# Optimization experiments

Measured on AMD Instinct MI355X. Metric: run time of the kernel, lower is better.

Reference implementation:

```python
import jax, jax.numpy as jnp
import numpy as np

B, S, E, H, L = 4, 8192, 1024, 16, 64
D = E // H

def setup_inputs() -> dict:
    key = jax.random.key(0)
    ks = jax.random.split(key, 8)
    scale = 1.0 / np.sqrt(E)
    inp = {
        'query': jax.random.normal(ks[0], (B, S, E), jnp.float32),
        'key':   jax.random.normal(ks[1], (B, S, E), jnp.float32),
        'value': jax.random.normal(ks[2], (B, S, E), jnp.float32),
        'Wq': jax.random.normal(ks[3], (E, E), jnp.float32) * scale,
        'bq': jnp.zeros((E,), jnp.float32),
        'Wk': jax.random.normal(ks[4], (E, E), jnp.float32) * scale,
        'bk': jnp.zeros((E,), jnp.float32),
        'Wv': jax.random.normal(ks[5], (E, E), jnp.float32) * scale,
        'bv': jnp.zeros((E,), jnp.float32),
        'Wo': jax.random.normal(ks[6], (E, E), jnp.float32) * scale,
        'bo': jnp.zeros((E,), jnp.float32),
    }
    return inp

def reference(query, key, value, Wq, bq, Wk, bk, Wv, bv, Wo, bo):
    b, s, _ = query.shape
    # projections (torch Linear: x @ W.T + b), split heads -> [B, H, S, D]
    def split(x):
        return x.reshape(b, s, H, D).transpose(0, 2, 1, 3)
    q = split(query @ Wq.T + bq)
    k = split(key   @ Wk.T + bk)
    v = split(value @ Wv.T + bv)
    # landmark selection: key-norms averaged over heads -> [B, S], topk L per batch
    scores = jnp.linalg.norm(k, axis=-1).mean(axis=1)        # [B, S]
    _, idx = jax.lax.top_k(scores, L)                        # [B, L]
    # gather landmark K/V -> [B, H, L, D]
    gidx = idx[:, None, :, None]                             # [B, 1, L, 1]
    k_sp = jnp.take_along_axis(k, gidx, axis=2)
    v_sp = jnp.take_along_axis(v, gidx, axis=2)
    # attention over landmarks only
    attn = jnp.einsum('bhsd,bhld->bhsl', q, k_sp) / jnp.sqrt(jnp.asarray(D, q.dtype))
    w = jax.nn.softmax(attn, axis=-1)                        # [B, H, S, L]
    out = jnp.einsum('bhsl,bhld->bhsd', w, v_sp)             # [B, H, S, D]
    out = out.transpose(0, 2, 1, 3).reshape(b, s, E)
    out = out @ Wo.T + bo
    return (out, w)
```

## Files before the change

### kernel.cpp

```cpp
#include <hip/hip_runtime.h>
#include <cstdint>

typedef unsigned short u16;
typedef __attribute__((ext_vector_type(8))) short short8;
typedef __attribute__((ext_vector_type(4))) float f32x4;

#define AS1 __attribute__((address_space(1)))
#define AS3 __attribute__((address_space(3)))

#define BB 4
#define SS 8192
#define EE 1024
#define HH 16
#define DD 64
#define LL 64
#define CANDN 96

__device__ __forceinline__ void async16(const void* g, void* l) {
  __builtin_amdgcn_global_load_lds((const AS1 uint32_t*)g, (AS3 uint32_t*)l, 16, 0, 0);
}
__device__ __forceinline__ u16 f2b(float f) {
  uint32_t u = __float_as_uint(f);
  return (u16)((u + 0x7fffu + ((u >> 16) & 1u)) >> 16);
}
__device__ __forceinline__ float b2f(u16 h) { return __uint_as_float(((uint32_t)h) << 16); }

__global__ __launch_bounds__(256) void cvt_bf16_k(const float* __restrict__ in, u16* __restrict__ out, int n4) {
  int i = blockIdx.x * 256 + threadIdx.x;
  if (i >= n4) return;
  float4 v = ((const float4*)in)[i];
  ushort4 o;
  o.x = f2b(v.x); o.y = f2b(v.y); o.z = f2b(v.z); o.w = f2b(v.w);
  ((ushort4*)out)[i] = o;
}

__global__ __launch_bounds__(256) void gemm_bt(const u16* __restrict__ A, const u16* __restrict__ W,
                                               const float* __restrict__ bias,
                                               float* __restrict__ Cf, u16* __restrict__ Cb, int K) {
  __shared__ __align__(16) u16 lA[4096];
  __shared__ __align__(16) u16 lB[4096];
  const int tid = threadIdx.x;
  const int wv = tid >> 6, lane = tid & 63;
  const int quad = lane >> 4, l15 = lane & 15;
  const int wm = wv >> 1, wn = wv & 1;

  const int nwg = gridDim.x * gridDim.y;
  int g = blockIdx.y * gridDim.x + blockIdx.x;
  int bx = blockIdx.x, by = blockIdx.y;
  if ((nwg & 7) == 0) {
    const int chunk = nwg >> 3;
    const int v = (g & 7) * chunk + (g >> 3);
    bx = v % gridDim.x;
    by = v / gridDim.x;
  }
  const int mt = by * 128, nt = bx * 128;

  const int row0 = tid >> 2, cg0 = (tid & 3) ^ ((row0 >> 1) & 3);
  const int row1 = (256 + tid) >> 2, cg1 = (tid & 3) ^ ((row1 >> 1) & 3);
  const u16* gA0 = A + (size_t)(mt + row0) * K + cg0 * 8;
  const u16* gA1 = A + (size_t)(mt + row1) * K + cg1 * 8;
  const u16* gB0 = W + (size_t)(nt + row0) * K + cg0 * 8;
  const u16* gB1 = W + (size_t)(nt + row1) * K + cg1 * 8;
  u16* lA0 = lA + tid * 8;  u16* lA1 = lA + 2048 + tid * 8;
  u16* lB0 = lB + tid * 8;  u16* lB1 = lB + 2048 + tid * 8;

  f32x4 acc[4][4];
#pragma unroll
  for (int i = 0; i < 4; i++)
#pragma unroll
    for (int j = 0; j < 4; j++) acc[i][j] = (f32x4){0.f, 0.f, 0.f, 0.f};

  const int am = 64 * wm + l15;
  const int bn = 64 * wn + l15;

  for (int kt = 0; kt < K; kt += 32) {
    async16(gA0 + kt, lA0);
    async16(gA1 + kt, lA1);
    async16(gB0 + kt, lB0);
    async16(gB1 + kt, lB1);
    __syncthreads();
    short8 af[4], bfr[4];
#pragma unroll
    for (int i = 0; i < 4; i++) {
      int r = am + 16 * i;
      af[i] = ((const short8*)lA)[r * 4 + (quad ^ ((r >> 1) & 3))];
      int rn = bn + 16 * i;
      bfr[i] = ((const short8*)lB)[rn * 4 + (quad ^ ((rn >> 1) & 3))];
    }
#pragma unroll
    for (int i = 0; i < 4; i++)
#pragma unroll
      for (int j = 0; j < 4; j++)
        acc[i][j] = __builtin_amdgcn_mfma_f32_16x16x32_bf16(af[i], bfr[j], acc[i][j], 0, 0, 0);
    __syncthreads();
  }

#pragma unroll
  for (int j = 0; j < 4; j++) {
    int gn = nt + 64 * wn + 16 * j + l15;
    float bs = bias[gn];
#pragma unroll
    for (int i = 0; i < 4; i++) {
#pragma unroll
      for (int r = 0; r < 4; r++) {
        int gm = mt + 64 * wm + 16 * i + quad * 4 + r;
        float v = acc[i][j][r] + bs;
        if (Cf) Cf[(size_t)gm * EE + gn] = v;
        if (Cb) Cb[(size_t)gm * EE + gn] = f2b(v);
      }
    }
  }
}

__global__ __launch_bounds__(256) void scores_k(const u16* __restrict__ kb, float* __restrict__ sc) {
  const int row = blockIdx.x;
  const int wv = threadIdx.x >> 6, lane = threadIdx.x & 63;
  __shared__ float part[4];
  float acc = 0.f;
  const u16* base = kb + (size_t)row * EE;
#pragma unroll
  for (int hh = 0; hh < 4; hh++) {
    float v = b2f(base[(wv * 4 + hh) * 64 + lane]);
    float s = v * v;
#pragma unroll
    for (int m = 1; m < 64; m <<= 1) s += __shfl_xor(s, m, 64);
    acc += sqrtf(s);
  }
  if (lane == 0) part[wv] = acc;
  __syncthreads();
  if (threadIdx.x == 0) sc[row] = (part[0] + part[1] + part[2] + part[3]) * (1.f / 16.f);
}

#define TKT 1024
#define EQCAP 256
__global__ __launch_bounds__(TKT) void topk1_k(const float* __restrict__ sc, int* __restrict__ cand) {
  const int b = blockIdx.x;
  __shared__ uint32_t s[SS];
  __shared__ int wsum[TKT / 64];
  __shared__ int cnt_sh;
  __shared__ int counter, eqcount;
  __shared__ int eqbuf[EQCAP];
  const int tid = threadIdx.x;
  const int lane = tid & 63, wv = tid >> 6;
  for (int i = tid; i < SS; i += TKT) s[i] = __float_as_uint(sc[b * SS + i]);
  if (tid == 0) { counter = 0; eqcount = 0; }
  __syncthreads();

  uint32_t lo = 0u, hi = 0x7f7fffffu;
  while (lo < hi) {
    uint32_t mid = lo + ((hi - lo + 1) >> 1);
    int c = 0;
    for (int i = tid; i < SS; i += TKT) c += (s[i] >= mid) ? 1 : 0;
#pragma unroll
    for (int m = 1; m < 64; m <<= 1) c += __shfl_xor(c, m, 64);
    if (lane == 0) wsum[wv] = c;
    __syncthreads();
    if (tid == 0) {
      int t = 0;
#pragma unroll
      for (int w = 0; w < TKT / 64; w++) t += wsum[w];
      cnt_sh = t;
    }
    __syncthreads();
    if (cnt_sh >= CANDN) lo = mid; else hi = mid - 1;
    __syncthreads();
  }
  const uint32_t T = lo;

  for (int i = tid; i < SS; i += TKT) {
    uint32_t u = s[i];
    if (u > T) {
      int p = atomicAdd(&counter, 1);
      cand[b * CANDN + p] = i;
    } else if (u == T) {
      int p = atomicAdd(&eqcount, 1);
      if (p < EQCAP) eqbuf[p] = i;
    }
  }
  __syncthreads();
  const int above = counter;
  const int rem = CANDN - above;
  int ec = eqcount; if (ec > EQCAP) ec = EQCAP;
  __syncthreads();
  for (int i = tid; i < ec; i += TKT) {
    int me = eqbuf[i];
    int rank = 0;
    for (int j = 0; j < ec; j++) rank += (eqbuf[j] < me) ? 1 : 0;
    if (rank < rem) {
      int p = atomicAdd(&counter, 1);
      cand[b * CANDN + p] = me;
    }
  }
}

__global__ __launch_bounds__(256) void rescore_k(const float* __restrict__ key, const float* __restrict__ Wk,
                                                 const int* __restrict__ cand, double* __restrict__ kpart) {
  const int kc = blockIdx.x, h = blockIdx.y, b = blockIdx.z;
  const int d = threadIdx.x & 63, cg = threadIdx.x >> 6;
  __shared__ float wk[64 * 257];
  __shared__ float xs[24 * 256];
  for (int i = threadIdx.x; i < 64 * 256; i += 256)
    wk[(i >> 8) * 257 + (i & 255)] = Wk[(size_t)(h * 64 + (i >> 8)) * EE + kc * 256 + (i & 255)];
  for (int c0 = 0; c0 < CANDN; c0 += 24) {
    __syncthreads();
    for (int i = threadIdx.x; i < 24 * 256; i += 256) {
      int c = c0 + (i >> 8);
      xs[i] = key[((size_t)b * SS + cand[b * CANDN + c]) * EE + kc * 256 + (i & 255)];
    }
    __syncthreads();
    double acc[6] = {0, 0, 0, 0, 0, 0};
    for (int kk = 0; kk < 256; kk++) {
      double wv_ = (double)wk[d * 257 + kk];
#pragma unroll
      for (int j = 0; j < 6; j++)
        acc[j] += wv_ * (double)xs[(cg * 6 + j) * 256 + kk];
    }
#pragma unroll
    for (int j = 0; j < 6; j++) {
      int c = c0 + cg * 6 + j;
      kpart[(((size_t)kc * BB + b) * CANDN + c) * 1024 + h * 64 + d] = acc[j];
    }
  }
}

__global__ __launch_bounds__(64) void score2_k(const double* __restrict__ kpart, const float* __restrict__ bk,
                                               double* __restrict__ sc2) {
  const int c = blockIdx.x, b = blockIdx.y;
  const int lane = threadIdx.x;
  double tot = 0.0;
  for (int h = 0; h < HH; h++) {
    double v = (double)bk[h * 64 + lane];
#pragma unroll
    for (int kc = 0; kc < 4; kc++)
      v += kpart[(((size_t)kc * BB + b) * CANDN + c) * 1024 + h * 64 + lane];
    double s = v * v;
#pragma unroll
    for (int m = 1; m < 64; m <<= 1) s += __shfl_xor(s, m, 64);
    tot += sqrt(s);
  }
  if (lane == 0) sc2[b * CANDN + c] = tot * (1.0 / 16.0);
}

__global__ __launch_bounds__(128) void topk2_k(const double* __restrict__ sc2, const int* __restrict__ cand,
                                               int* __restrict__ idxf) {
  const int b = blockIdx.x, t = threadIdx.x;
  if (t >= CANDN) return;
  double my = sc2[b * CANDN + t];
  int mi = cand[b * CANDN + t];
  int rank = 0;
  for (int j = 0; j < CANDN; j++) {
    double sj = sc2[b * CANDN + j];
    int ij = cand[b * CANDN + j];
    if (sj > my || (sj == my && ij < mi)) rank++;
  }
  if (rank < LL) idxf[b * LL + rank] = mi;
}

__global__ __launch_bounds__(256) void gatherx_k(const float* __restrict__ value, const int* __restrict__ idxf,
                                                 u16* __restrict__ xg) {
  const int r = blockIdx.x;
  const int b = r >> 6;
  const float* src = value + ((size_t)b * SS + idxf[r]) * EE;
  for (int i = threadIdx.x; i < EE; i += 256) xg[(size_t)r * EE + i] = f2b(src[i]);
}

__global__ __launch_bounds__(64) void gathersp_k(const u16* __restrict__ kb, const float* __restrict__ vg,
                                                 const int* __restrict__ idxf,
                                                 u16* __restrict__ ksp, u16* __restrict__ vspT) {
  const int g = blockIdx.x;
  const int l = g & 63, h = (g >> 6) & 15, b = g >> 10;
  const int d = threadIdx.x;
  ksp[(size_t)g * 64 + d] = kb[((size_t)b * SS + idxf[b * 64 + l]) * EE + h * 64 + d];
  vspT[((size_t)(b * 16 + h) * 64 + d) * 64 + l] = f2b(vg[((size_t)b * 64 + l) * EE + h * 64 + d]);
}

__global__ __launch_bounds__(256) void attn_k(const u16* __restrict__ qb, const u16* __restrict__ ksp,
                                              const u16* __restrict__ vspT,
                                              float* __restrict__ wout, u16* __restrict__ attnb) {
  __shared__ __align__(16) u16 qt[4096];
  __shared__ __align__(16) u16 kt[4096];
  __shared__ __align__(16) u16 vt[4096];
  __shared__ __align__(16) u16 wt[4096];
  const int tid = threadIdx.x;
  const int wv = tid >> 6, lane = tid & 63, quad = lane >> 4, l15 = lane & 15;
  const int s0 = blockIdx.x * 64;
  const int bh = blockIdx.y, b = bh >> 4, h = bh & 15;

  {
    const int bi0 = tid, bi1 = 256 + tid;
    const int r0 = bi0 >> 3, c0 = (bi0 & 7) ^ (r0 & 7);
    const int r1 = bi1 >> 3, c1 = (bi1 & 7) ^ (r1 & 7);
    const u16* qg = qb + ((size_t)b * SS + s0) * EE + h * 64;
    async16(qg + (size_t)r0 * EE + c0 * 8, qt + bi0 * 8);
    async16(qg + (size_t)r1 * EE + c1 * 8, qt + bi1 * 8);
    const u16* kg = ksp + (size_t)bh * 4096;
    async16(kg + r0 * 64 + c0 * 8, kt + bi0 * 8);
    async16(kg + r1 * 64 + c1 * 8, kt + bi1 * 8);
    const u16* vgp = vspT + (size_t)bh * 4096;
    async16(vgp + r0 * 64 + c0 * 8, vt + bi0 * 8);
    async16(vgp + r1 * 64 + c1 * 8, vt + bi1 * 8);
  }
  __syncthreads();

  f32x4 acc[4];
#pragma unroll
  for (int j = 0; j < 4; j++) acc[j] = (f32x4){0.f, 0.f, 0.f, 0.f};
  const int ar = 16 * wv + l15;
#pragma unroll
  for (int ks = 0; ks < 2; ks++) {
    const int cg = quad + ks * 4;
    short8 af = ((const short8*)qt)[ar * 8 + (cg ^ (ar & 7))];
#pragma unroll
    for (int j = 0; j < 4; j++) {
      int br = 16 * j + l15;
      short8 bf = ((const short8*)kt)[br * 8 + (cg ^ (br & 7))];
      acc[j] = __builtin_amdgcn_mfma_f32_16x16x32_bf16(af, bf, acc[j], 0, 0, 0);
    }
  }
#pragma unroll
  for (int j = 0; j < 4; j++) acc[j] *= 0.125f;

  float inv[4];
#pragma unroll
  for (int r = 0; r < 4; r++) {
    float m = fmaxf(fmaxf(acc[0][r], acc[1][r]), fmaxf(acc[2][r], acc[3][r]));
#pragma unroll
    for (int msk = 1; msk < 16; msk <<= 1) m = fmaxf(m, __shfl_xor(m, msk, 64));
    float e0 = __expf(acc[0][r] - m);
    float e1 = __expf(acc[1][r] - m);
    float e2 = __expf(acc[2][r] - m);
    float e3 = __expf(acc[3][r] - m);
    acc[0][r] = e0; acc[1][r] = e1; acc[2][r] = e2; acc[3][r] = e3;
    float s = e0 + e1 + e2 + e3;
#pragma unroll
    for (int msk = 1; msk < 16; msk <<= 1) s += __shfl_xor(s, msk, 64);
    inv[r] = 1.f / s;
  }

  const size_t wbase = ((size_t)bh * SS + s0 + 16 * wv) * 64;
#pragma unroll
  for (int j = 0; j < 4; j++) {
#pragma unroll
    for (int r = 0; r < 4; r++) {
      float val = acc[j][r] * inv[r];
      int rowl = quad * 4 + r;
      int l = 16 * j + l15;
      wout[wbase + (size_t)rowl * 64 + l] = val;
      int wr = 16 * wv + rowl;
      wt[wr * 64 + ((l >> 3) ^ (wr & 7)) * 8 + (l & 7)] = f2b(val);
    }
  }
  __syncthreads();

  f32x4 acc2[4];
#pragma unroll
  for (int j = 0; j < 4; j++) acc2[j] = (f32x4){0.f, 0.f, 0.f, 0.f};
#pragma unroll
  for (int ks = 0; ks < 2; ks++) {
    const int cg = quad + ks * 4;
    short8 af = ((const short8*)wt)[ar * 8 + (cg ^ (ar & 7))];
#pragma unroll
    for (int j = 0; j < 4; j++) {
      int br = 16 * j + l15;
      short8 bf = ((const short8*)vt)[br * 8 + (cg ^ (br & 7))];
      acc2[j] = __builtin_amdgcn_mfma_f32_16x16x32_bf16(af, bf, acc2[j], 0, 0, 0);
    }
  }
#pragma unroll
  for (int j = 0; j < 4; j++)
#pragma unroll
    for (int r = 0; r < 4; r++)
      attnb[((size_t)b * SS + s0 + 16 * wv + quad * 4 + r) * EE + h * 64 + 16 * j + l15] = f2b(acc2[j][r]);
}

extern "C" void kernel_launch(void* const* d_in, const int* in_sizes, int n_in,
                              void* d_out, int out_size, void* d_ws, size_t ws_size,
                              hipStream_t stream) {
  (void)in_sizes; (void)n_in; (void)out_size; (void)ws_size;
  const float* query = (const float*)d_in[0];
  const float* key   = (const float*)d_in[1];
  const float* value = (const float*)d_in[2];
  const float* Wq = (const float*)d_in[3];
  const float* bq = (const float*)d_in[4];
  const float* Wk = (const float*)d_in[5];
  const float* bk = (const float*)d_in[6];
  const float* Wv = (const float*)d_in[7];
  const float* bv = (const float*)d_in[8];
  const float* Wo = (const float*)d_in[9];
  const float* bo = (const float*)d_in[10];
  float* out = (float*)d_out;
  float* wout = out + (size_t)BB * SS * EE;

  char* p = (char*)d_ws;
  auto alloc = [&](size_t n) { char* r = p; p += (n + 255) & ~(size_t)255; return r; };
  u16* qbf = (u16*)alloc((size_t)BB * SS * EE * 2);
  u16* kbf = (u16*)alloc((size_t)BB * SS * EE * 2);
  u16* wqb = (u16*)alloc((size_t)EE * EE * 2);
  u16* wkb = (u16*)alloc((size_t)EE * EE * 2);
  u16* wvb = (u16*)alloc((size_t)EE * EE * 2);
  u16* wob = (u16*)alloc((size_t)EE * EE * 2);
  u16* qb  = (u16*)alloc((size_t)BB * SS * EE * 2);
  u16* kb  = (u16*)alloc((size_t)BB * SS * EE * 2);
  float*  sc    = (float*)alloc((size_t)BB * SS * 4);
  int*    cand  = (int*)alloc(BB * CANDN * 4);
  double* kpart = (double*)alloc((size_t)4 * BB * CANDN * 1024 * 8);
  double* sc2   = (double*)alloc(BB * CANDN * 8);
  int*    idxf  = (int*)alloc(BB * LL * 4);
  u16*    xg    = (u16*)alloc((size_t)BB * LL * EE * 2);
  float*  vg    = (float*)alloc((size_t)BB * LL * EE * 4);
  u16*    ksp   = (u16*)alloc((size_t)BB * HH * LL * DD * 2);
  u16*    vspT  = (u16*)alloc((size_t)BB * HH * DD * LL * 2);
  u16*    attnb = qbf;

  const int M = BB * SS;

  cvt_bf16_k<<<(M * EE / 4 + 255) / 256, 256, 0, stream>>>(query, qbf, M * EE / 4);
  cvt_bf16_k<<<(M * EE / 4 + 255) / 256, 256, 0, stream>>>(key, kbf, M * EE / 4);
  cvt_bf16_k<<<(EE * EE / 4 + 255) / 256, 256, 0, stream>>>(Wq, wqb, EE * EE / 4);
  cvt_bf16_k<<<(EE * EE / 4 + 255) / 256, 256, 0, stream>>>(Wk, wkb, EE * EE / 4);
  cvt_bf16_k<<<(EE * EE / 4 + 255) / 256, 256, 0, stream>>>(Wv, wvb, EE * EE / 4);
  cvt_bf16_k<<<(EE * EE / 4 + 255) / 256, 256, 0, stream>>>(Wo, wob, EE * EE / 4);

  dim3 gg(EE / 128, M / 128);
  gemm_bt<<<gg, 256, 0, stream>>>(qbf, wqb, bq, nullptr, qb, EE);
  gemm_bt<<<gg, 256, 0, stream>>>(kbf, wkb, bk, nullptr, kb, EE);

  scores_k<<<M, 256, 0, stream>>>(kb, sc);
  topk1_k<<<BB, TKT, 0, stream>>>(sc, cand);
  rescore_k<<<dim3(4, HH, BB), 256, 0, stream>>>(key, Wk, cand, kpart);
  score2_k<<<dim3(CANDN, BB), 64, 0, stream>>>(kpart, bk, sc2);
  topk2_k<<<BB, 128, 0, stream>>>(sc2, cand, idxf);

  gatherx_k<<<BB * LL, 256, 0, stream>>>(value, idxf, xg);
  gemm_bt<<<dim3(EE / 128, BB * LL / 128), 256, 0, stream>>>(xg, wvb, bv, vg, nullptr, EE);
  gathersp_k<<<BB * HH * LL, 64, 0, stream>>>(kb, vg, idxf, ksp, vspT);

  attn_k<<<dim3(SS / 64, BB * HH), 256, 0, stream>>>(qb, ksp, vspT, wout, attnb);

  gemm_bt<<<gg, 256, 0, stream>>>(attnb, wob, bo, out, nullptr, EE);
}
```

Baseline: 1.077 ms.

## Replace GEMM with double-buffered 256x128 tile, 512-thread, K64 pipelined kernel

New measurement: 1.006 ms. 1.07x faster.

```diff
diff --git a/kernel.cpp b/kernel.cpp
--- a/kernel.cpp
+++ b/kernel.cpp
@@ -34,11 +34,16 @@
   ((ushort4*)out)[i] = o;
 }
 
-__global__ __launch_bounds__(256) void gemm_bt(const u16* __restrict__ A, const u16* __restrict__ W,
+#define FENCE_RW()  asm volatile("s_waitcnt lgkmcnt(0)\n\ts_barrier" ::: "memory")
+#define FENCE_V6()  asm volatile("s_waitcnt vmcnt(6)\n\ts_barrier" ::: "memory")
+#define FENCE_V0()  asm volatile("s_waitcnt vmcnt(0)\n\ts_barrier" ::: "memory")
+
+__global__ __launch_bounds__(512) void gemm256(const u16* __restrict__ A, const u16* __restrict__ W,
                                                const float* __restrict__ bias,
                                                float* __restrict__ Cf, u16* __restrict__ Cb, int K) {
-  __shared__ __align__(16) u16 lA[4096];
-  __shared__ __align__(16) u16 lB[4096];
+  extern __shared__ __align__(16) u16 lds_[];
+  u16* lA = lds_;
+  u16* lB = lds_ + 32768;
   const int tid = threadIdx.x;
   const int wv = tid >> 6, lane = tid & 63;
   const int quad = lane >> 4, l15 = lane & 15;
@@ -53,16 +58,28 @@
     bx = v % gridDim.x;
     by = v / gridDim.x;
   }
-  const int mt = by * 128, nt = bx * 128;
-
-  const int row0 = tid >> 2, cg0 = (tid & 3) ^ ((row0 >> 1) & 3);
-  const int row1 = (256 + tid) >> 2, cg1 = (tid & 3) ^ ((row1 >> 1) & 3);
-  const u16* gA0 = A + (size_t)(mt + row0) * K + cg0 * 8;
-  const u16* gA1 = A + (size_t)(mt + row1) * K + cg1 * 8;
-  const u16* gB0 = W + (size_t)(nt + row0) * K + cg0 * 8;
-  const u16* gB1 = W + (size_t)(nt + row1) * K + cg1 * 8;
-  u16* lA0 = lA + tid * 8;  u16* lA1 = lA + 2048 + tid * 8;
-  u16* lB0 = lB + tid * 8;  u16* lB1 = lB + 2048 + tid * 8;
+  const int mt = by * 256, nt = bx * 128;
+
+  const int rl = tid >> 3;
+  const int g8 = (((tid & 7) ^ (rl & 7))) * 8;
+  const u16* sA00 = A + (size_t)(mt + rl) * K + g8;
+  const u16* sA01 = A + (size_t)(mt + 64 + rl) * K + g8;
+  const u16* sA10 = A + (size_t)(mt + 128 + rl) * K + g8;
+  const u16* sA11 = A + (size_t)(mt + 192 + rl) * K + g8;
+  const u16* sB0  = W + (size_t)(nt + rl) * K + g8;
+  const u16* sB1  = W + (size_t)(nt + 64 + rl) * K + g8;
+  const int dA = tid * 8;
+  const int dB = tid * 8;
+
+  auto STAGE = [&](int tile, int pb) {
+    const int off = tile * 64;
+    async16(sA00 + off, lA + pb * 16384 + dA);
+    async16(sA01 + off, lA + pb * 16384 + dA + 4096);
+    async16(sA10 + off, lA + pb * 16384 + 8192 + dA);
+    async16(sA11 + off, lA + pb * 16384 + 8192 + dA + 4096);
+    async16(sB0 + off, lB + pb * 8192 + dB);
+    async16(sB1 + off, lB + pb * 8192 + dB + 4096);
+  };
 
   f32x4 acc[4][4];
 #pragma unroll
@@ -70,29 +87,40 @@
 #pragma unroll
     for (int j = 0; j < 4; j++) acc[i][j] = (f32x4){0.f, 0.f, 0.f, 0.f};
 
-  const int am = 64 * wm + l15;
-  const int bn = 64 * wn + l15;
-
-  for (int kt = 0; kt < K; kt += 32) {
-    async16(gA0 + kt, lA0);
-    async16(gA1 + kt, lA1);
-    async16(gB0 + kt, lB0);
-    async16(gB1 + kt, lB1);
-    __syncthreads();
-    short8 af[4], bfr[4];
+  const int NT = K >> 6;
+  STAGE(0, 0);
+  STAGE(1, 1);
+  FENCE_V6();
+
+  for (int t = 0; t < NT; ++t) {
+    const int pb = t & 1;
+    const short8* pA = (const short8*)(lA + pb * 16384);
+    const short8* pB = (const short8*)(lB + pb * 8192);
+    short8 af[2][4], bf[2][4];
 #pragma unroll
     for (int i = 0; i < 4; i++) {
-      int r = am + 16 * i;
-      af[i] = ((const short8*)lA)[r * 4 + (quad ^ ((r >> 1) & 3))];
-      int rn = bn + 16 * i;
-      bfr[i] = ((const short8*)lB)[rn * 4 + (quad ^ ((rn >> 1) & 3))];
+      const int r = 64 * wm + 16 * i + l15;
+      af[0][i] = pA[r * 8 + (quad ^ (r & 7))];
+      af[1][i] = pA[r * 8 + ((quad + 4) ^ (r & 7))];
+      const int rb = 64 * wn + 16 * i + l15;
+      bf[0][i] = pB[rb * 8 + (quad ^ (rb & 7))];
+      bf[1][i] = pB[rb * 8 + ((quad + 4) ^ (rb & 7))];
     }
 #pragma unroll
     for (int i = 0; i < 4; i++)
 #pragma unroll
       for (int j = 0; j < 4; j++)
-        acc[i][j] = __builtin_amdgcn_mfma_f32_16x16x32_bf16(af[i], bfr[j], acc[i][j], 0, 0, 0);
-    __syncthreads();
+        acc[i][j] = __builtin_amdgcn_mfma_f32_16x16x32_bf16(af[0][i], bf[0][j], acc[i][j], 0, 0, 0);
+    FENCE_RW();
+    if (t + 2 < NT) STAGE(t + 2, pb);
+#pragma unroll
+    for (int i = 0; i < 4; i++)
+#pragma unroll
+      for (int j = 0; j < 4; j++)
+        acc[i][j] = __builtin_amdgcn_mfma_f32_16x16x32_bf16(af[1][i], bf[1][j], acc[i][j], 0, 0, 0);
+    if (t + 1 < NT) {
+      if (t + 1 == NT - 1) { FENCE_V0(); } else { FENCE_V6(); }
+    }
   }
 
 #pragma unroll
@@ -413,6 +441,7 @@
   u16*    attnb = qbf;
 
   const int M = BB * SS;
+  const size_t gemm_lds = 98304;
 
   cvt_bf16_k<<<(M * EE / 4 + 255) / 256, 256, 0, stream>>>(query, qbf, M * EE / 4);
   cvt_bf16_k<<<(M * EE / 4 + 255) / 256, 256, 0, stream>>>(key, kbf, M * EE / 4);
@@ -421,9 +450,9 @@
   cvt_bf16_k<<<(EE * EE / 4 + 255) / 256, 256, 0, stream>>>(Wv, wvb, EE * EE / 4);
   cvt_bf16_k<<<(EE * EE / 4 + 255) / 256, 256, 0, stream>>>(Wo, wob, EE * EE / 4);
 
-  dim3 gg(EE / 128, M / 128);
-  gemm_bt<<<gg, 256, 0, stream>>>(qbf, wqb, bq, nullptr, qb, EE);
-  gemm_bt<<<gg, 256, 0, stream>>>(kbf, wkb, bk, nullptr, kb, EE);
+  dim3 gg(EE / 128, M / 256);
+  gemm256<<<gg, 512, gemm_lds, stream>>>(qbf, wqb, bq, nullptr, qb, EE);
+  gemm256<<<gg, 512, gemm_lds, stream>>>(kbf, wkb, bk, nullptr, kb, EE);
 
   scores_k<<<M, 256, 0, stream>>>(kb, sc);
   topk1_k<<<BB, TKT, 0, stream>>>(sc, cand);
@@ -432,10 +461,10 @@
   topk2_k<<<BB, 128, 0, stream>>>(sc2, cand, idxf);
 
   gatherx_k<<<BB * LL, 256, 0, stream>>>(value, idxf, xg);
-  gemm_bt<<<dim3(EE / 128, BB * LL / 128), 256, 0, stream>>>(xg, wvb, bv, vg, nullptr, EE);
+  gemm256<<<dim3(EE / 128, BB * LL / 256), 512, gemm_lds, stream>>>(xg, wvb, bv, vg, nullptr, EE);
   gathersp_k<<<BB * HH * LL, 64, 0, stream>>>(kb, vg, idxf, ksp, vspT);
 
   attn_k<<<dim3(SS / 64, BB * HH), 256, 0, stream>>>(qb, ksp, vspT, wout, attnb);
 
-  gemm_bt<<<gg, 256, 0, stream>>>(attnb, wob, bo, out, nullptr, EE);
-}
+  gemm256<<<gg, 512, gemm_lds, stream>>>(attnb, wob, bo, out, nullptr, EE);
+}
```
